# Kernel tuning notes

Hardware: AMD Instinct MI355X
Metric: run time of the kernel (lower is better)

Reference implementation:

```python
import jax, jax.numpy as jnp
from jax import lax
import numpy as np

INPUT_SIZE, HIDDEN, NUM_LAYERS, OUTPUT = 64, 512, 2, 1024
BATCH, SEQ = 64, 1024


def setup_inputs() -> dict:
    key = jax.random.key(0)
    ks = jax.random.split(key, 11)
    s = 1.0 / np.sqrt(HIDDEN)
    u = lambda k, shape: jax.random.uniform(k, shape, jnp.float32, -s, s)
    return {
        "x": jax.random.normal(ks[0], (BATCH, SEQ, INPUT_SIZE), jnp.float32),
        # layer 0 (PyTorch gate order: i, f, g, o stacked along dim 0)
        "W_ih0": u(ks[1], (4 * HIDDEN, INPUT_SIZE)),
        "W_hh0": u(ks[2], (4 * HIDDEN, HIDDEN)),
        "b_ih0": u(ks[3], (4 * HIDDEN,)),
        "b_hh0": u(ks[4], (4 * HIDDEN,)),
        # layer 1
        "W_ih1": u(ks[5], (4 * HIDDEN, HIDDEN)),
        "W_hh1": u(ks[6], (4 * HIDDEN, HIDDEN)),
        "b_ih1": u(ks[7], (4 * HIDDEN,)),
        "b_hh1": u(ks[8], (4 * HIDDEN,)),
        # fc
        "fc_w": u(ks[9], (OUTPUT, HIDDEN)),
        "fc_b": u(ks[10], (OUTPUT,)),
    }


def _lstm_layer(x, W_ih, W_hh, b_ih, b_hh):
    # x: [B, T, D]. Precompute input projection for all timesteps (one big GEMM).
    B = x.shape[0]
    H = W_hh.shape[1]
    xw = jnp.einsum('btd,gd->btg', x, W_ih) + b_ih + b_hh  # [B, T, 4H]
    xw = jnp.swapaxes(xw, 0, 1)  # [T, B, 4H] for scan
    h0 = jnp.zeros((B, H), x.dtype)
    c0 = jnp.zeros((B, H), x.dtype)

    def step(carry, xw_t):
        h, c = carry
        gates = xw_t + h @ W_hh.T  # [B, 4H]
        i, f, g, o = jnp.split(gates, 4, axis=-1)
        c = jax.nn.sigmoid(f) * c + jax.nn.sigmoid(i) * jnp.tanh(g)
        h = jax.nn.sigmoid(o) * jnp.tanh(c)
        return (h, c), h

    (h_T, c_T), hs = lax.scan(step, (h0, c0), xw)
    return jnp.swapaxes(hs, 0, 1), h_T  # [B, T, H], [B, H]


def _forward(x, W_ih0, W_hh0, b_ih0, b_hh0, W_ih1, W_hh1, b_ih1, b_hh1, fc_w, fc_b):
    ula0, h0_T = _lstm_layer(x, W_ih0, W_hh0, b_ih0, b_hh0)
    ula1, h1_T = _lstm_layer(ula0, W_ih1, W_hh1, b_ih1, b_hh1)
    # h_out: [num_layers, B, H] -> view(-1, H)
    h_out = jnp.concatenate([h0_T, h1_T], axis=0)  # [L*B, H]
    out = h_out @ fc_w.T + fc_b
    out = jax.nn.relu(out)
    # Dropout(p=0.2): identity in eval mode (deterministic reference)
    return out


def reference(x, W_ih0, W_hh0, b_ih0, b_hh0, W_ih1, W_hh1, b_ih1, b_hh1, fc_w, fc_b):
    return _forward(x, W_ih0, W_hh0, b_ih0, b_hh0, W_ih1, W_hh1, b_ih1, b_hh1, fc_w, fc_b)
```

## Files before the change

### kernel.cpp

```cpp
#include <hip/hip_runtime.h>


#define H      512
#define T_SEQ  1024
#define DIN    64

#define D0       5
#define D1       3
#define H0_SLOT  8192
#define H1_OFF   40960
#define PROG_OFF 65536
#define GRP_U32  65792
#define WS_BYTES (4 * GRP_U32 * 4)

typedef _Float16 f16x8 __attribute__((ext_vector_type(8)));
typedef float    f32x4 __attribute__((ext_vector_type(4)));
typedef unsigned long long u64t;

__device__ __forceinline__ u64t ld_u64(const u64t* p) {
  return __hip_atomic_load((u64t*)p, __ATOMIC_RELAXED, __HIP_MEMORY_SCOPE_AGENT);
}
__device__ __forceinline__ unsigned ld_u32a(const unsigned* p) {
  return __hip_atomic_load((unsigned*)p, __ATOMIC_RELAXED, __HIP_MEMORY_SCOPE_AGENT);
}
__device__ __forceinline__ void st_u32(unsigned* p, unsigned v) {
  __hip_atomic_store(p, v, __ATOMIC_RELAXED, __HIP_MEMORY_SCOPE_AGENT);
}
__device__ __forceinline__ f16x8 pk8(float4 a, float4 b) {
  f16x8 r;
  r[0] = (_Float16)a.x; r[1] = (_Float16)a.y; r[2] = (_Float16)a.z; r[3] = (_Float16)a.w;
  r[4] = (_Float16)b.x; r[5] = (_Float16)b.y; r[6] = (_Float16)b.z; r[7] = (_Float16)b.w;
  return r;
}
__device__ __forceinline__ f16x8 cvt8(const float* p) {
  return pk8(*(const float4*)p, *(const float4*)(p + 4));
}
__device__ __forceinline__ f32x4 mfma16(f16x8 a, f16x8 b, f32x4 c) {
  return __builtin_amdgcn_mfma_f32_16x16x32_f16(a, b, c, 0, 0, 0);
}
__device__ __forceinline__ float rcpf_(float x) {
#if __has_builtin(__builtin_amdgcn_rcpf)
  return __builtin_amdgcn_rcpf(x);
#else
  return 1.0f / x;
#endif
}
__device__ __forceinline__ float sigm(float x) {
  x = fminf(fmaxf(x, -30.f), 30.f);
  return rcpf_(1.f + __expf(-x));
}
__device__ __forceinline__ float tanhx(float x) {
  x = fminf(fmaxf(x, -15.f), 15.f);
  float e = __expf(2.f * x);
  return (e - 1.f) * rcpf_(e + 1.f);
}
__device__ __forceinline__ unsigned payload(u64t v) {
  return ((unsigned)v & 0xffffu) | ((unsigned)(v >> 32) << 16);
}

__global__ __launch_bounds__(256, 1)
void lstm_fused(const float* __restrict__ x,
                const float* __restrict__ Wih0, const float* __restrict__ Whh0,
                const float* __restrict__ bih0, const float* __restrict__ bhh0,
                const float* __restrict__ Wih1, const float* __restrict__ Whh1,
                const float* __restrict__ bih1, const float* __restrict__ bhh1,
                const float* __restrict__ fcw,  const float* __restrict__ fcb,
                float* __restrict__ out, unsigned* __restrict__ ws)
{
  __shared__ unsigned sH[2 * 8320];

  const int tid  = threadIdx.x;
  const int r    = blockIdx.x;
  const int g    = blockIdx.y;
  const int wv   = tid >> 6;
  const int lane = tid & 63;
  const int bcol = lane & 15;
  const int kgrp = lane >> 4;
  const bool isL0 = (r < 16);

  unsigned* gbase = ws + g * GRP_U32;
  unsigned* prog  = gbase + PROG_OFF;

  const int src_m = lane & 15;
  const int hb = isL0 ? (r * 32 + wv * 8) : ((r - 16) * 16 + wv * 4);
  const int gr0 = (src_m & 3) * H + hb + (src_m >> 2);

  f16x8 wA[36];
  if (isL0) {
    const int gr1 = gr0 + 4;
    #pragma unroll
    for (int f = 0; f < 18; ++f) {
      const float *p0, *p1;
      if (f < 2) {
        p0 = Wih0 + (size_t)gr0 * DIN + f * 32 + kgrp * 8;
        p1 = Wih0 + (size_t)gr1 * DIN + f * 32 + kgrp * 8;
      } else {
        p0 = Whh0 + (size_t)gr0 * H + (f - 2) * 32 + kgrp * 8;
        p1 = Whh0 + (size_t)gr1 * H + (f - 2) * 32 + kgrp * 8;
      }
      wA[f] = cvt8(p0); wA[18 + f] = cvt8(p1);
    }
  } else {
    #pragma unroll
    for (int f = 0; f < 16; ++f)
      wA[f] = cvt8(Wih1 + (size_t)gr0 * H + f * 32 + kgrp * 8);
    #pragma unroll
    for (int f = 0; f < 16; ++f)
      wA[16 + f] = cvt8(Whh1 + (size_t)gr0 * H + f * 32 + kgrp * 8);
  }
  float bias0[4], bias1[4];
  {
    const float* bi = isL0 ? bih0 : bih1;
    const float* bh = isL0 ? bhh0 : bhh1;
    #pragma unroll
    for (int rr = 0; rr < 4; ++rr) {
      int u0 = hb + kgrp;
      bias0[rr] = bi[rr * H + u0] + bh[rr * H + u0];
      int u1 = hb + 4 + kgrp;
      bias1[rr] = isL0 ? (bi[rr * H + u1] + bh[rr * H + u1]) : 0.f;
    }
  }

  for (int i = tid; i < 2 * 8320; i += 256) sH[i] = 0;
  __syncthreads();

  unsigned spins = 0;
  const int rowb = bcol * 1040 + kgrp * 16;

  if (isL0) {
    float c0 = 0.f, c1 = 0.f;
    for (int t = 0; t < T_SEQ; ++t) {
      const float* xp = x + ((size_t)((g * 16 + bcol) * T_SEQ + t)) * DIN + kgrp * 8;
      float4 xr0 = *(const float4*)xp;        float4 xr1 = *(const float4*)(xp + 4);
      float4 xr2 = *(const float4*)(xp + 32); float4 xr3 = *(const float4*)(xp + 36);
      if (t > 0) {
        const u64t* src = (const u64t*)(gbase + ((t - 1) % D0) * H0_SLOT);
        const unsigned want = (unsigned)t;
        u64t v[16];
        #pragma unroll
        for (int i = 0; i < 16; ++i) v[i] = ld_u64(src + tid + i * 256);
        for (;;) {
          unsigned bad = 0;
          #pragma unroll
          for (int i = 0; i < 16; ++i) {
            unsigned lo = (unsigned)v[i], hi = (unsigned)(v[i] >> 32);
            if (((lo >> 16) ^ want) | ((hi >> 16) ^ want)) bad |= (1u << i);
          }
          if (!bad) break;
          if (++spins > 4000000u) break;
          #pragma unroll
          for (int i = 0; i < 16; ++i)
            if (bad & (1u << i)) v[i] = ld_u64(src + tid + i * 256);
        }
        if (wv == 0) {
          int pv = (lane < 32) ? (int)ld_u32a(prog + lane) : 0x7fffffff;
          while (!__all(pv >= t - 4)) {
            if (++spins > 4000000u) break;
            if (lane < 32) pv = (int)ld_u32a(prog + lane);
          }
        }
        unsigned* db = sH + (t & 1) * 8320;
        #pragma unroll
        for (int i = 0; i < 16; ++i) {
          int j = tid + i * 256;
          db[(j >> 8) * 260 + (j & 255)] = payload(v[i]);
        }
      }
      __syncthreads();

      const char* cur = (const char*)(sH + (t & 1) * 8320);
      f32x4 a0 = {0,0,0,0}, a1 = {0,0,0,0};
      {
        f16x8 b0 = pk8(xr0, xr1);
        a0 = mfma16(wA[0], b0, a0); a1 = mfma16(wA[18], b0, a1);
        f16x8 b1 = pk8(xr2, xr3);
        a0 = mfma16(wA[1], b1, a0); a1 = mfma16(wA[19], b1, a1);
      }
      #pragma unroll
      for (int f = 2; f < 18; ++f) {
        f16x8 bf = *(const f16x8*)(cur + rowb + (f - 2) * 64);
        a0 = mfma16(wA[f], bf, a0); a1 = mfma16(wA[18 + f], bf, a1);
      }
      float hv0, hv1;
      {
        float ii = sigm(a0[0] + bias0[0]);
        float ff = sigm(a0[1] + bias0[1]);
        float gg = tanhx(a0[2] + bias0[2]);
        float oo = sigm(a0[3] + bias0[3]);
        c0 = ff * c0 + ii * gg;  hv0 = oo * tanhx(c0);
      }
      {
        float ii = sigm(a1[0] + bias1[0]);
        float ff = sigm(a1[1] + bias1[1]);
        float gg = tanhx(a1[2] + bias1[2]);
        float oo = sigm(a1[3] + bias1[3]);
        c1 = ff * c1 + ii * gg;  hv1 = oo * tanhx(c1);
      }
      unsigned tag = (unsigned)(t + 1) << 16;
      unsigned u0 = (unsigned)__builtin_bit_cast(unsigned short, (_Float16)hv0);
      unsigned u1 = (unsigned)__builtin_bit_cast(unsigned short, (_Float16)hv1);
      unsigned* dst = gbase + (t % D0) * H0_SLOT + bcol * 512 + hb + kgrp;
      st_u32(dst,     u0 | tag);
      st_u32(dst + 4, u1 | tag);
    }
  } else {
    const int q = r - 16;
    float c0 = 0.f;
    for (int u = 0; u < T_SEQ; ++u) {
      const u64t* s0 = (const u64t*)(gbase + (u % D0) * H0_SLOT);
      const u64t* s1 = (const u64t*)(gbase + H1_OFF + ((u + 2) % D1) * H0_SLOT);
      const unsigned w0 = (unsigned)(u + 1), w1 = (unsigned)u;
      u64t v0[16], v1[16];
      #pragma unroll
      for (int i = 0; i < 16; ++i) v0[i] = ld_u64(s0 + tid + i * 256);
      if (u > 0) {
        #pragma unroll
        for (int i = 0; i < 16; ++i) v1[i] = ld_u64(s1 + tid + i * 256);
      }
      for (;;) {
        unsigned bad0 = 0, bad1 = 0;
        #pragma unroll
        for (int i = 0; i < 16; ++i) {
          unsigned lo = (unsigned)v0[i], hi = (unsigned)(v0[i] >> 32);
          if (((lo >> 16) ^ w0) | ((hi >> 16) ^ w0)) bad0 |= (1u << i);
        }
        if (u > 0) {
          #pragma unroll
          for (int i = 0; i < 16; ++i) {
            unsigned lo = (unsigned)v1[i], hi = (unsigned)(v1[i] >> 32);
            if (((lo >> 16) ^ w1) | ((hi >> 16) ^ w1)) bad1 |= (1u << i);
          }
        }
        if (!(bad0 | bad1)) break;
        if (++spins > 4000000u) break;
        #pragma unroll
        for (int i = 0; i < 16; ++i) {
          if (bad0 & (1u << i)) v0[i] = ld_u64(s0 + tid + i * 256);
          if (bad1 & (1u << i)) v1[i] = ld_u64(s1 + tid + i * 256);
        }
      }
      unsigned* db = sH + (u & 1) * 8320;
      #pragma unroll
      for (int i = 0; i < 16; ++i) {
        int j = tid + i * 256;
        db[(j >> 8) * 260 + (j & 255)] = payload(v0[i]);
      }
      if (u > 0) {
        #pragma unroll
        for (int i = 0; i < 16; ++i) {
          int j = tid + i * 256;
          db[4160 + (j >> 8) * 260 + (j & 255)] = payload(v1[i]);
        }
      }
      __syncthreads();
      if (tid == 0) st_u32(prog + q, (unsigned)(u + 1));

      const char* cur = (const char*)db;
      f32x4 a0 = {0,0,0,0}, a1 = {0,0,0,0};
      #pragma unroll
      for (int f = 0; f < 16; ++f) {
        f16x8 bf = *(const f16x8*)(cur + rowb + f * 64);
        if (f & 1) a1 = mfma16(wA[f], bf, a1); else a0 = mfma16(wA[f], bf, a0);
      }
      #pragma unroll
      for (int f = 0; f < 16; ++f) {
        f16x8 bf = *(const f16x8*)(cur + 16640 + rowb + f * 64);
        if (f & 1) a1 = mfma16(wA[16 + f], bf, a1); else a0 = mfma16(wA[16 + f], bf, a0);
      }
      f32x4 a = a0 + a1;
      float ii = sigm(a[0] + bias0[0]);
      float ff = sigm(a[1] + bias0[1]);
      float gg = tanhx(a[2] + bias0[2]);
      float oo = sigm(a[3] + bias0[3]);
      c0 = ff * c0 + ii * gg;
      float hv = oo * tanhx(c0);

      unsigned tag = (unsigned)(u + 1) << 16;
      unsigned hu = (unsigned)__builtin_bit_cast(unsigned short, (_Float16)hv);
      unsigned* dst = gbase + H1_OFF + (u % D1) * H0_SLOT + bcol * 512 + hb + kgrp;
      st_u32(dst, hu | tag);
    }
  }

  const int fid = g * 48 + r;
  if (fid < 128) {
    const int rt = fid >> 4, ct = fid & 15;
    const int sg = rt & 3;
    const bool isH1 = (rt >= 4);
    const u64t* src = (const u64t*)(ws + sg * GRP_U32
                                    + (isH1 ? (H1_OFF + 0 * H0_SLOT) : (3 * H0_SLOT)));
    const unsigned want = (unsigned)T_SEQ;
    u64t v[16];
    #pragma unroll
    for (int i = 0; i < 16; ++i) v[i] = ld_u64(src + tid + i * 256);
    for (;;) {
      unsigned bad = 0;
      #pragma unroll
      for (int i = 0; i < 16; ++i) {
        unsigned lo = (unsigned)v[i], hi = (unsigned)(v[i] >> 32);
        if (((lo >> 16) ^ want) | ((hi >> 16) ^ want)) bad |= (1u << i);
      }
      if (!bad) break;
      if (++spins > 4000000u) break;
      __builtin_amdgcn_s_sleep(1);
      #pragma unroll
      for (int i = 0; i < 16; ++i)
        if (bad & (1u << i)) v[i] = ld_u64(src + tid + i * 256);
    }
    __syncthreads();
    #pragma unroll
    for (int i = 0; i < 16; ++i) {
      int j = tid + i * 256;
      sH[(j >> 8) * 260 + (j & 255)] = payload(v[i]);
    }
    __syncthreads();
    const int col = ct * 64 + wv * 16 + bcol;
    f32x4 a0 = {0,0,0,0}, a1 = {0,0,0,0};
    #pragma unroll
    for (int f = 0; f < 16; ++f) {
      f16x8 af = *(const f16x8*)((const char*)sH + rowb + f * 64);
      f16x8 bf = cvt8(fcw + (size_t)col * H + f * 32 + kgrp * 8);
      if (f & 1) a1 = mfma16(af, bf, a1); else a0 = mfma16(af, bf, a0);
    }
    f32x4 a = a0 + a1;
    const float fb = fcb[col];
    #pragma unroll
    for (int rr = 0; rr < 4; ++rr) {
      int row = rt * 16 + kgrp * 4 + rr;
      float v2 = a[rr] + fb;
      out[(size_t)row * 1024 + col] = v2 > 0.f ? v2 : 0.f;
    }
  }
}

extern "C" void kernel_launch(void* const* d_in, const int* in_sizes, int n_in,
                              void* d_out, int out_size, void* d_ws, size_t ws_size,
                              hipStream_t stream) {
  const float* x    = (const float*)d_in[0];
  const float* Wih0 = (const float*)d_in[1];
  const float* Whh0 = (const float*)d_in[2];
  const float* bih0 = (const float*)d_in[3];
  const float* bhh0 = (const float*)d_in[4];
  const float* Wih1 = (const float*)d_in[5];
  const float* Whh1 = (const float*)d_in[6];
  const float* bih1 = (const float*)d_in[7];
  const float* bhh1 = (const float*)d_in[8];
  const float* fcw  = (const float*)d_in[9];
  const float* fcb  = (const float*)d_in[10];
  (void)in_sizes; (void)n_in; (void)out_size; (void)ws_size;

  hipMemsetAsync(d_ws, 0, WS_BYTES, stream);
  lstm_fused<<<dim3(48, 4), dim3(256), 0, stream>>>(
      x, Wih0, Whh0, bih0, bhh0, Wih1, Whh1, bih1, bhh1, fcw, fcb,
      (float*)d_out, (unsigned*)d_ws);
}
```

Measured before the change: 4.539 ms.

## Lockstep both LSTM layers in a unified wavefront loop with fewer, larger blocks

```diff
diff --git a/kernel.cpp b/kernel.cpp
--- a/kernel.cpp
+++ b/kernel.cpp
@@ -4,13 +4,10 @@
 #define H      512
 #define T_SEQ  1024
 #define DIN    64
-
-#define D0       5
-#define D1       3
-#define H0_SLOT  8192
-#define H1_OFF   40960
-#define PROG_OFF 65536
-#define GRP_U32  65792
+#define STEPS  1025
+
+#define SLOT_U32 16384
+#define GRP_U32  49152
 #define WS_BYTES (4 * GRP_U32 * 4)
 
 typedef _Float16 f16x8 __attribute__((ext_vector_type(8)));
@@ -20,10 +17,10 @@
 __device__ __forceinline__ u64t ld_u64(const u64t* p) {
   return __hip_atomic_load((u64t*)p, __ATOMIC_RELAXED, __HIP_MEMORY_SCOPE_AGENT);
 }
-__device__ __forceinline__ unsigned ld_u32a(const unsigned* p) {
-  return __hip_atomic_load((unsigned*)p, __ATOMIC_RELAXED, __HIP_MEMORY_SCOPE_AGENT);
-}
 __device__ __forceinline__ void st_u32(unsigned* p, unsigned v) {
+  __hip_atomic_store(p, v, __ATOMIC_RELAXED, __HIP_MEMORY_SCOPE_AGENT);
+}
+__device__ __forceinline__ void st_u64(u64t* p, u64t v) {
   __hip_atomic_store(p, v, __ATOMIC_RELAXED, __HIP_MEMORY_SCOPE_AGENT);
 }
 __device__ __forceinline__ f16x8 pk8(float4 a, float4 b) {
@@ -58,7 +55,7 @@
   return ((unsigned)v & 0xffffu) | ((unsigned)(v >> 32) << 16);
 }
 
-__global__ __launch_bounds__(256, 1)
+__global__ __launch_bounds__(512, 1)
 void lstm_fused(const float* __restrict__ x,
                 const float* __restrict__ Wih0, const float* __restrict__ Whh0,
                 const float* __restrict__ bih0, const float* __restrict__ bhh0,
@@ -76,18 +73,17 @@
   const int lane = tid & 63;
   const int bcol = lane & 15;
   const int kgrp = lane >> 4;
-  const bool isL0 = (r < 16);
+  const bool isL0 = (r < 8);
 
   unsigned* gbase = ws + g * GRP_U32;
-  unsigned* prog  = gbase + PROG_OFF;
 
   const int src_m = lane & 15;
-  const int hb = isL0 ? (r * 32 + wv * 8) : ((r - 16) * 16 + wv * 4);
-  const int gr0 = (src_m & 3) * H + hb + (src_m >> 2);
+  const int hb = isL0 ? (r * 64 + wv * 8) : ((r - 8) * 32 + wv * 4);
 
   f16x8 wA[36];
   if (isL0) {
-    const int gr1 = gr0 + 4;
+    const int gr0 = (src_m & 3) * H + hb + 2 * (src_m >> 2);
+    const int gr1 = gr0 + 1;
     #pragma unroll
     for (int f = 0; f < 18; ++f) {
       const float *p0, *p1;
@@ -101,6 +97,7 @@
       wA[f] = cvt8(p0); wA[18 + f] = cvt8(p1);
     }
   } else {
+    const int gr0 = (src_m & 3) * H + hb + (src_m >> 2);
     #pragma unroll
     for (int f = 0; f < 16; ++f)
       wA[f] = cvt8(Wih1 + (size_t)gr0 * H + f * 32 + kgrp * 8);
@@ -112,209 +109,161 @@
   {
     const float* bi = isL0 ? bih0 : bih1;
     const float* bh = isL0 ? bhh0 : bhh1;
+    const int u0 = isL0 ? (hb + 2 * kgrp) : (hb + kgrp);
+    const int u1 = isL0 ? (hb + 2 * kgrp + 1) : 0;
     #pragma unroll
     for (int rr = 0; rr < 4; ++rr) {
-      int u0 = hb + kgrp;
       bias0[rr] = bi[rr * H + u0] + bh[rr * H + u0];
-      int u1 = hb + 4 + kgrp;
       bias1[rr] = isL0 ? (bi[rr * H + u1] + bh[rr * H + u1]) : 0.f;
     }
   }
 
-  for (int i = tid; i < 2 * 8320; i += 256) sH[i] = 0;
+  for (int i = tid; i < 2 * 8320; i += 512) sH[i] = 0;
   __syncthreads();
 
+  float c0 = 0.f, c1 = 0.f;
   unsigned spins = 0;
   const int rowb = bcol * 1040 + kgrp * 16;
 
-  if (isL0) {
-    float c0 = 0.f, c1 = 0.f;
-    for (int t = 0; t < T_SEQ; ++t) {
+  for (int s = 0; s < STEPS; ++s) {
+    if (s > 0) {
+      const u64t* src = (const u64t*)(gbase + ((s - 1) % 3) * SLOT_U32);
+      const unsigned want = (unsigned)s;
+      u64t v[16];
+      #pragma unroll
+      for (int i = 0; i < 16; ++i) v[i] = ld_u64(src + tid + i * 512);
+      for (;;) {
+        unsigned bad = 0;
+        #pragma unroll
+        for (int i = 0; i < 16; ++i) {
+          unsigned lo = (unsigned)v[i], hi = (unsigned)(v[i] >> 32);
+          if (((lo >> 16) ^ want) | ((hi >> 16) ^ want)) bad |= (1u << i);
+        }
+        if (!bad) break;
+        if (++spins > 8000000u) break;
+        #pragma unroll
+        for (int i = 0; i < 16; ++i)
+          if (bad & (1u << i)) v[i] = ld_u64(src + tid + i * 512);
+      }
+      unsigned* db = sH + (s & 1) * 8320;
+      #pragma unroll
+      for (int i = 0; i < 16; ++i) {
+        int j = tid + i * 512;
+        db[(j >> 12) * 4160 + ((j >> 8) & 15) * 260 + (j & 255)] = payload(v[i]);
+      }
+    }
+    float4 xr0 = {0,0,0,0}, xr1 = xr0, xr2 = xr0, xr3 = xr0;
+    if (isL0) {
+      int t = (s < T_SEQ) ? s : (T_SEQ - 1);
       const float* xp = x + ((size_t)((g * 16 + bcol) * T_SEQ + t)) * DIN + kgrp * 8;
-      float4 xr0 = *(const float4*)xp;        float4 xr1 = *(const float4*)(xp + 4);
-      float4 xr2 = *(const float4*)(xp + 32); float4 xr3 = *(const float4*)(xp + 36);
-      if (t > 0) {
-        const u64t* src = (const u64t*)(gbase + ((t - 1) % D0) * H0_SLOT);
-        const unsigned want = (unsigned)t;
-        u64t v[16];
-        #pragma unroll
-        for (int i = 0; i < 16; ++i) v[i] = ld_u64(src + tid + i * 256);
-        for (;;) {
-          unsigned bad = 0;
-          #pragma unroll
-          for (int i = 0; i < 16; ++i) {
-            unsigned lo = (unsigned)v[i], hi = (unsigned)(v[i] >> 32);
-            if (((lo >> 16) ^ want) | ((hi >> 16) ^ want)) bad |= (1u << i);
-          }
-          if (!bad) break;
-          if (++spins > 4000000u) break;
-          #pragma unroll
-          for (int i = 0; i < 16; ++i)
-            if (bad & (1u << i)) v[i] = ld_u64(src + tid + i * 256);
-        }
-        if (wv == 0) {
-          int pv = (lane < 32) ? (int)ld_u32a(prog + lane) : 0x7fffffff;
-          while (!__all(pv >= t - 4)) {
-            if (++spins > 4000000u) break;
-            if (lane < 32) pv = (int)ld_u32a(prog + lane);
-          }
-        }
-        unsigned* db = sH + (t & 1) * 8320;
-        #pragma unroll
-        for (int i = 0; i < 16; ++i) {
-          int j = tid + i * 256;
-          db[(j >> 8) * 260 + (j & 255)] = payload(v[i]);
-        }
-      }
-      __syncthreads();
-
-      const char* cur = (const char*)(sH + (t & 1) * 8320);
-      f32x4 a0 = {0,0,0,0}, a1 = {0,0,0,0};
-      {
+      xr0 = *(const float4*)xp;        xr1 = *(const float4*)(xp + 4);
+      xr2 = *(const float4*)(xp + 32); xr3 = *(const float4*)(xp + 36);
+    }
+    __syncthreads();
+
+    const bool act = isL0 ? (s < T_SEQ) : (s > 0);
+    const char* cur = (const char*)(sH + (s & 1) * 8320);
+    if (isL0) {
+      float hv0 = 0.f, hv1 = 0.f;
+      if (act) {
+        f32x4 a0 = {0,0,0,0}, a1 = {0,0,0,0};
         f16x8 b0 = pk8(xr0, xr1);
         a0 = mfma16(wA[0], b0, a0); a1 = mfma16(wA[18], b0, a1);
         f16x8 b1 = pk8(xr2, xr3);
         a0 = mfma16(wA[1], b1, a0); a1 = mfma16(wA[19], b1, a1);
-      }
-      #pragma unroll
-      for (int f = 2; f < 18; ++f) {
-        f16x8 bf = *(const f16x8*)(cur + rowb + (f - 2) * 64);
-        a0 = mfma16(wA[f], bf, a0); a1 = mfma16(wA[18 + f], bf, a1);
-      }
-      float hv0, hv1;
+        #pragma unroll
+        for (int f = 2; f < 18; ++f) {
+          f16x8 bf = *(const f16x8*)(cur + rowb + (f - 2) * 64);
+          a0 = mfma16(wA[f], bf, a0); a1 = mfma16(wA[18 + f], bf, a1);
+        }
+        {
+          float ii = sigm(a0[0] + bias0[0]);
+          float ff = sigm(a0[1] + bias0[1]);
+          float gg = tanhx(a0[2] + bias0[2]);
+          float oo = sigm(a0[3] + bias0[3]);
+          c0 = ff * c0 + ii * gg;  hv0 = oo * tanhx(c0);
+        }
+        {
+          float ii = sigm(a1[0] + bias1[0]);
+          float ff = sigm(a1[1] + bias1[1]);
+          float gg = tanhx(a1[2] + bias1[2]);
+          float oo = sigm(a1[3] + bias1[3]);
+          c1 = ff * c1 + ii * gg;  hv1 = oo * tanhx(c1);
+        }
+      }
+      if (s < T_SEQ) {
+        u64t tag = (u64t)((unsigned)(s + 1) << 16);
+        u64t w0 = tag | (u64t)(unsigned short)__builtin_bit_cast(unsigned short, (_Float16)hv0);
+        u64t w1 = tag | (u64t)(unsigned short)__builtin_bit_cast(unsigned short, (_Float16)hv1);
+        u64t* dst = (u64t*)(gbase + (s % 3) * SLOT_U32 + bcol * 512 + hb) + kgrp;
+        st_u64(dst, w0 | (w1 << 32));
+      }
+    } else {
+      float hv = 0.f;
+      if (act) {
+        f32x4 a0 = {0,0,0,0}, a1 = {0,0,0,0};
+        #pragma unroll
+        for (int f = 0; f < 16; ++f) {
+          f16x8 bf = *(const f16x8*)(cur + rowb + f * 64);
+          if (f & 1) a1 = mfma16(wA[f], bf, a1); else a0 = mfma16(wA[f], bf, a0);
+        }
+        #pragma unroll
+        for (int f = 0; f < 16; ++f) {
+          f16x8 bf = *(const f16x8*)(cur + 16640 + rowb + f * 64);
+          if (f & 1) a1 = mfma16(wA[16 + f], bf, a1); else a0 = mfma16(wA[16 + f], bf, a0);
+        }
+        f32x4 a = a0 + a1;
+        float ii = sigm(a[0] + bias0[0]);
+        float ff = sigm(a[1] + bias0[1]);
+        float gg = tanhx(a[2] + bias0[2]);
+        float oo = sigm(a[3] + bias0[3]);
+        c0 = ff * c0 + ii * gg;
+        hv = oo * tanhx(c0);
+      }
       {
-        float ii = sigm(a0[0] + bias0[0]);
-        float ff = sigm(a0[1] + bias0[1]);
-        float gg = tanhx(a0[2] + bias0[2]);
-        float oo = sigm(a0[3] + bias0[3]);
-        c0 = ff * c0 + ii * gg;  hv0 = oo * tanhx(c0);
-      }
-      {
-        float ii = sigm(a1[0] + bias1[0]);
-        float ff = sigm(a1[1] + bias1[1]);
-        float gg = tanhx(a1[2] + bias1[2]);
-        float oo = sigm(a1[3] + bias1[3]);
-        c1 = ff * c1 + ii * gg;  hv1 = oo * tanhx(c1);
-      }
-      unsigned tag = (unsigned)(t + 1) << 16;
-      unsigned u0 = (unsigned)__builtin_bit_cast(unsigned short, (_Float16)hv0);
-      unsigned u1 = (unsigned)__builtin_bit_cast(unsigned short, (_Float16)hv1);
-      unsigned* dst = gbase + (t % D0) * H0_SLOT + bcol * 512 + hb + kgrp;
-      st_u32(dst,     u0 | tag);
-      st_u32(dst + 4, u1 | tag);
-    }
-  } else {
-    const int q = r - 16;
-    float c0 = 0.f;
-    for (int u = 0; u < T_SEQ; ++u) {
-      const u64t* s0 = (const u64t*)(gbase + (u % D0) * H0_SLOT);
-      const u64t* s1 = (const u64t*)(gbase + H1_OFF + ((u + 2) % D1) * H0_SLOT);
-      const unsigned w0 = (unsigned)(u + 1), w1 = (unsigned)u;
-      u64t v0[16], v1[16];
-      #pragma unroll
-      for (int i = 0; i < 16; ++i) v0[i] = ld_u64(s0 + tid + i * 256);
-      if (u > 0) {
-        #pragma unroll
-        for (int i = 0; i < 16; ++i) v1[i] = ld_u64(s1 + tid + i * 256);
-      }
-      for (;;) {
-        unsigned bad0 = 0, bad1 = 0;
-        #pragma unroll
-        for (int i = 0; i < 16; ++i) {
-          unsigned lo = (unsigned)v0[i], hi = (unsigned)(v0[i] >> 32);
-          if (((lo >> 16) ^ w0) | ((hi >> 16) ^ w0)) bad0 |= (1u << i);
-        }
-        if (u > 0) {
-          #pragma unroll
-          for (int i = 0; i < 16; ++i) {
-            unsigned lo = (unsigned)v1[i], hi = (unsigned)(v1[i] >> 32);
-            if (((lo >> 16) ^ w1) | ((hi >> 16) ^ w1)) bad1 |= (1u << i);
-          }
-        }
-        if (!(bad0 | bad1)) break;
-        if (++spins > 4000000u) break;
-        #pragma unroll
-        for (int i = 0; i < 16; ++i) {
-          if (bad0 & (1u << i)) v0[i] = ld_u64(s0 + tid + i * 256);
-          if (bad1 & (1u << i)) v1[i] = ld_u64(s1 + tid + i * 256);
-        }
-      }
-      unsigned* db = sH + (u & 1) * 8320;
-      #pragma unroll
-      for (int i = 0; i < 16; ++i) {
-        int j = tid + i * 256;
-        db[(j >> 8) * 260 + (j & 255)] = payload(v0[i]);
-      }
-      if (u > 0) {
-        #pragma unroll
-        for (int i = 0; i < 16; ++i) {
-          int j = tid + i * 256;
-          db[4160 + (j >> 8) * 260 + (j & 255)] = payload(v1[i]);
-        }
-      }
-      __syncthreads();
-      if (tid == 0) st_u32(prog + q, (unsigned)(u + 1));
-
-      const char* cur = (const char*)db;
-      f32x4 a0 = {0,0,0,0}, a1 = {0,0,0,0};
-      #pragma unroll
-      for (int f = 0; f < 16; ++f) {
-        f16x8 bf = *(const f16x8*)(cur + rowb + f * 64);
-        if (f & 1) a1 = mfma16(wA[f], bf, a1); else a0 = mfma16(wA[f], bf, a0);
-      }
-      #pragma unroll
-      for (int f = 0; f < 16; ++f) {
-        f16x8 bf = *(const f16x8*)(cur + 16640 + rowb + f * 64);
-        if (f & 1) a1 = mfma16(wA[16 + f], bf, a1); else a0 = mfma16(wA[16 + f], bf, a0);
-      }
-      f32x4 a = a0 + a1;
-      float ii = sigm(a[0] + bias0[0]);
-      float ff = sigm(a[1] + bias0[1]);
-      float gg = tanhx(a[2] + bias0[2]);
-      float oo = sigm(a[3] + bias0[3]);
-      c0 = ff * c0 + ii * gg;
-      float hv = oo * tanhx(c0);
-
-      unsigned tag = (unsigned)(u + 1) << 16;
-      unsigned hu = (unsigned)__builtin_bit_cast(unsigned short, (_Float16)hv);
-      unsigned* dst = gbase + H1_OFF + (u % D1) * H0_SLOT + bcol * 512 + hb + kgrp;
-      st_u32(dst, hu | tag);
+        unsigned tag = (unsigned)(s + 1) << 16;
+        unsigned hu = (unsigned)__builtin_bit_cast(unsigned short, (_Float16)hv);
+        unsigned* dst = gbase + (s % 3) * SLOT_U32 + 8192 + bcol * 512 + hb + kgrp;
+        st_u32(dst, hu | tag);
+      }
     }
   }
 
-  const int fid = g * 48 + r;
-  if (fid < 128) {
-    const int rt = fid >> 4, ct = fid & 15;
+  __syncthreads();
+
+  const int fid = g * 24 + r;
+  if (fid < 64) {
+    const int rt = fid >> 3;
     const int sg = rt & 3;
     const bool isH1 = (rt >= 4);
-    const u64t* src = (const u64t*)(ws + sg * GRP_U32
-                                    + (isH1 ? (H1_OFF + 0 * H0_SLOT) : (3 * H0_SLOT)));
-    const unsigned want = (unsigned)T_SEQ;
-    u64t v[16];
-    #pragma unroll
-    for (int i = 0; i < 16; ++i) v[i] = ld_u64(src + tid + i * 256);
+    const unsigned want = isH1 ? (unsigned)STEPS : (unsigned)(STEPS - 1);
+    const int     slot  = isH1 ? 1 : 0;
+    const u64t* src = (const u64t*)(ws + sg * GRP_U32 + slot * SLOT_U32
+                                    + (isH1 ? 8192 : 0));
+    u64t v[8];
+    #pragma unroll
+    for (int i = 0; i < 8; ++i) v[i] = ld_u64(src + tid + i * 512);
     for (;;) {
       unsigned bad = 0;
       #pragma unroll
-      for (int i = 0; i < 16; ++i) {
+      for (int i = 0; i < 8; ++i) {
         unsigned lo = (unsigned)v[i], hi = (unsigned)(v[i] >> 32);
         if (((lo >> 16) ^ want) | ((hi >> 16) ^ want)) bad |= (1u << i);
       }
       if (!bad) break;
-      if (++spins > 4000000u) break;
-      __builtin_amdgcn_s_sleep(1);
+      if (++spins > 8000000u) break;
       #pragma unroll
-      for (int i = 0; i < 16; ++i)
-        if (bad & (1u << i)) v[i] = ld_u64(src + tid + i * 256);
+      for (int i = 0; i < 8; ++i)
+        if (bad & (1u << i)) v[i] = ld_u64(src + tid + i * 512);
+    }
+    #pragma unroll
+    for (int i = 0; i < 8; ++i) {
+      int j = tid + i * 512;
+      sH[(j >> 8) * 260 + (j & 255)] = payload(v[i]);
     }
     __syncthreads();
-    #pragma unroll
-    for (int i = 0; i < 16; ++i) {
-      int j = tid + i * 256;
-      sH[(j >> 8) * 260 + (j & 255)] = payload(v[i]);
-    }
-    __syncthreads();
-    const int col = ct * 64 + wv * 16 + bcol;
+    const int ct  = (fid & 7) * 2 + (wv >> 2);
+    const int col = ct * 64 + (wv & 3) * 16 + bcol;
     f32x4 a0 = {0,0,0,0}, a1 = {0,0,0,0};
     #pragma unroll
     for (int f = 0; f < 16; ++f) {
@@ -350,7 +299,7 @@
   (void)in_sizes; (void)n_in; (void)out_size; (void)ws_size;
 
   hipMemsetAsync(d_ws, 0, WS_BYTES, stream);
-  lstm_fused<<<dim3(48, 4), dim3(256), 0, stream>>>(
+  lstm_fused<<<dim3(24, 4), dim3(512), 0, stream>>>(
       x, Wih0, Whh0, bih0, bhh0, Wih1, Whh1, bih1, bhh1, fcw, fcb,
       (float*)d_out, (unsigned*)d_ws);
 }
```

Result: slower. 6.058 ms (+33.5%).
